# Kernel tuning notes

Hardware: AMD Instinct MI355X
Metric: run time of the kernel (lower is better)

## Reference

```python
import jax, jax.numpy as jnp
import numpy as np

N_HEAD = 16

def setup_inputs() -> dict:
    key = jax.random.key(0)
    k1, k2, k3 = jax.random.split(key, 3)
    B, T, C = 4, 2048, 1024
    x = jax.random.normal(k1, (B, T, C), dtype=jnp.float32)
    W_attn = jax.random.normal(k2, (C, 3 * C), dtype=jnp.float32) * (1.0 / np.sqrt(C))
    b_attn = jnp.zeros((3 * C,), dtype=jnp.float32)
    W_proj = jax.random.normal(k3, (C, C), dtype=jnp.float32) * (1.0 / np.sqrt(C))
    b_proj = jnp.zeros((C,), dtype=jnp.float32)
    return {"x": x, "W_attn": W_attn, "b_attn": b_attn, "W_proj": W_proj, "b_proj": b_proj, "train": 0}

def reference(x, W_attn, b_attn, W_proj, b_proj, train):
    # Causal self-attention, eval mode (dropout = identity since dropout=0.0 / train=False).
    B, T, C = x.shape
    H = N_HEAD
    hd = C // H
    qkv = x @ W_attn + b_attn                      # [B, T, 3C]
    q, k, v = jnp.split(qkv, 3, axis=-1)
    def to_heads(a):
        return a.reshape(B, T, H, hd).swapaxes(1, 2)   # [B, H, T, hd]
    q, k, v = to_heads(q), to_heads(k), to_heads(v)
    scale = 1.0 / jnp.sqrt(jnp.asarray(hd, dtype=x.dtype))
    attn = jnp.einsum('bhqd,bhkd->bhqk', q, k) * scale   # [B, H, T, T]
    causal = jnp.tril(jnp.ones((T, T), dtype=bool))
    attn = jnp.where(causal, attn, -jnp.inf)
    p = jax.nn.softmax(attn, axis=-1)
    y = jnp.einsum('bhqk,bhkd->bhqd', p, v)              # [B, H, T, hd]
    y = y.swapaxes(1, 2).reshape(B, T, C)
    return y @ W_proj + b_proj
```

## Files before the change

### kernel.cpp

```cpp
#include <hip/hip_runtime.h>
#include <hip/hip_bf16.h>
#include <math.h>

typedef __attribute__((ext_vector_type(8))) short short8;
typedef __attribute__((ext_vector_type(4))) short short4v;
typedef __attribute__((ext_vector_type(4))) float floatx4;
using bf16 = __hip_bfloat16;

#define DEVI __device__ __forceinline__

DEVI floatx4 fzero4() { floatx4 z; z[0]=0.f; z[1]=0.f; z[2]=0.f; z[3]=0.f; return z; }

DEVI float ex2(float x) {
  float r;
  asm("v_exp_f32 %0, %1" : "=v"(r) : "v"(x));
  return r;
}

DEVI float max3f(float a, float b, float c) {
  float d;
  asm("v_max3_f32 %0, %1, %2, %3" : "=v"(d) : "v"(a), "v"(b), "v"(c));
  return d;
}

DEVI unsigned short f2b(float x) {
  union { bf16 h; unsigned short u; } c;
  c.h = __float2bfloat16(x);
  return c.u;
}

DEVI floatx4 mfma16(short4v a, short4v b, floatx4 c) {
#if __has_builtin(__builtin_amdgcn_mfma_f32_16x16x16bf16_1k)
  return __builtin_amdgcn_mfma_f32_16x16x16bf16_1k(a, b, c, 0, 0, 0);
#else
  floatx4 d;
  asm("v_mfma_f32_16x16x16_bf16 %0, %1, %2, %3" : "=v"(d) : "v"(a), "v"(b), "v"(c));
  return d;
#endif
}

DEVI void gload16(const bf16* g, bf16* l) {
  typedef __attribute__((address_space(1))) const void gv_t;
  typedef __attribute__((address_space(3))) void lv_t;
  __builtin_amdgcn_global_load_lds((gv_t*)g, (lv_t*)l, 16, 0, 0);
}

__global__ __launch_bounds__(256) void k_transpose(const float* __restrict__ in,
                                                   bf16* __restrict__ out,
                                                   int R, int C) {
  __shared__ float tile[32][33];
  int x = blockIdx.x * 32 + threadIdx.x;
  for (int i = threadIdx.y; i < 32; i += 8) {
    int y = blockIdx.y * 32 + i;
    tile[i][threadIdx.x] = (y < R && x < C) ? in[(size_t)y * C + x] : 0.f;
  }
  __syncthreads();
  int ox = blockIdx.y * 32 + threadIdx.x;
  for (int i = threadIdx.y; i < 32; i += 8) {
    int oy = blockIdx.x * 32 + i;
    if (oy < C && ox < R) out[(size_t)oy * R + ox] = __float2bfloat16(tile[threadIdx.x][i]);
  }
}

#define LOG2E_O8 0.18033688011112042f

__global__ __launch_bounds__(256) void k_gemmA(
    const float* __restrict__ Ax, const bf16* __restrict__ Bt,
    const float* __restrict__ bias,
    bf16* __restrict__ Qo, bf16* __restrict__ Ko, bf16* __restrict__ Vo) {
  __shared__ bf16 sA[2][128 * 32];
  __shared__ bf16 sB[2][128 * 32];
  const int Kd = 1024;
  const int tid = threadIdx.x;
  const int w = tid >> 6, l = tid & 63;
  const int lg = l >> 4, li = l & 15;
  const int wr = w >> 1, wc = w & 1;
  const int ii = blockIdx.x >> 3, xcd = blockIdx.x & 7;
  const int bx = ii >> 3, by = xcd * 8 + (ii & 7);
  const int m0 = by * 128, n0 = bx * 128;

  const int r0 = tid >> 2, ko0 = (tid & 3) * 8;
  const float* pax0 = Ax + (size_t)(m0 + r0) * Kd + ko0;
  const float* pax1 = Ax + (size_t)(m0 + 64 + r0) * Kd + ko0;
  const bf16* pb0 = Bt + (size_t)(n0 + r0) * Kd + ko0;
  const bf16* pb1 = Bt + (size_t)(n0 + 64 + r0) * Kd + ko0;

  floatx4 acc[4][4];
#pragma unroll
  for (int i = 0; i < 4; ++i)
#pragma unroll
    for (int j = 0; j < 4; ++j) acc[i][j] = fzero4();

  float4 va0, va1, va2, va3;

  auto ISSUE_A = [&](int k0) {
    va0 = *(const float4*)(pax0 + k0);
    va1 = *(const float4*)(pax0 + k0 + 4);
    va2 = *(const float4*)(pax1 + k0);
    va3 = *(const float4*)(pax1 + k0 + 4);
  };
  auto WRITE_A = [&](int buf) {
    short8 s0, s1;
    s0[0] = (short)f2b(va0.x); s0[1] = (short)f2b(va0.y);
    s0[2] = (short)f2b(va0.z); s0[3] = (short)f2b(va0.w);
    s0[4] = (short)f2b(va1.x); s0[5] = (short)f2b(va1.y);
    s0[6] = (short)f2b(va1.z); s0[7] = (short)f2b(va1.w);
    s1[0] = (short)f2b(va2.x); s1[1] = (short)f2b(va2.y);
    s1[2] = (short)f2b(va2.z); s1[3] = (short)f2b(va2.w);
    s1[4] = (short)f2b(va3.x); s1[5] = (short)f2b(va3.y);
    s1[6] = (short)f2b(va3.z); s1[7] = (short)f2b(va3.w);
    *(short8*)&sA[buf][r0 * 32 + ko0] = s0;
    *(short8*)&sA[buf][(64 + r0) * 32 + ko0] = s1;
  };
  auto STAGE_B = [&](int buf, int k0) {
    gload16(pb0 + k0, &sB[buf][w * 512]);
    gload16(pb1 + k0, &sB[buf][2048 + w * 512]);
  };

  ISSUE_A(0);
  STAGE_B(0, 0);
  WRITE_A(0);
  asm volatile("s_waitcnt lgkmcnt(0)" ::: "memory");

  int cur = 0;
  for (int k0 = 0; k0 < Kd; k0 += 32) {
    const int nxt = cur ^ 1;
    const bool pf = (k0 + 32 < Kd);
    if (pf) {
      ISSUE_A(k0 + 32);
      STAGE_B(nxt, k0 + 32);
      asm volatile("s_waitcnt vmcnt(6)" ::: "memory");
    } else {
      asm volatile("s_waitcnt vmcnt(0)" ::: "memory");
    }
    __builtin_amdgcn_s_barrier();
    short8 af[4], bfr[4];
#pragma unroll
    for (int i = 0; i < 4; ++i)
      af[i] = *(const short8*)&sA[cur][(wr * 64 + i * 16 + li) * 32 + lg * 8];
#pragma unroll
    for (int j = 0; j < 4; ++j)
      bfr[j] = *(const short8*)&sB[cur][(wc * 64 + j * 16 + li) * 32 + lg * 8];
#pragma unroll
    for (int i = 0; i < 4; ++i)
#pragma unroll
      for (int j = 0; j < 4; ++j)
        acc[i][j] = __builtin_amdgcn_mfma_f32_16x16x32_bf16(af[i], bfr[j], acc[i][j], 0, 0, 0);
    if (pf) {
      WRITE_A(nxt);
      asm volatile("s_waitcnt lgkmcnt(0)" ::: "memory");
    }
    __builtin_amdgcn_s_barrier();
    cur = nxt;
  }

#pragma unroll
  for (int i = 0; i < 4; ++i) {
#pragma unroll
    for (int j = 0; j < 4; ++j) {
      const int ng = n0 + wc * 64 + j * 16 + li;
      const float bs = bias[ng];
      const int mgb = m0 + wr * 64 + i * 16 + lg * 4;
      const int bb = mgb >> 11, t = mgb & 2047;
      const int d = ng & 63;
      if (ng < 1024) {
        const int h = ng >> 6;
#pragma unroll
        for (int r = 0; r < 4; ++r)
          Qo[(((size_t)bb * 16 + h) * 2048 + t + r) * 64 + d] =
              __float2bfloat16((acc[i][j][r] + bs) * LOG2E_O8);
      } else if (ng < 2048) {
        const int h = (ng - 1024) >> 6;
#pragma unroll
        for (int r = 0; r < 4; ++r)
          Ko[(((size_t)bb * 16 + h) * 2048 + t + r) * 64 + d] =
              __float2bfloat16(acc[i][j][r] + bs);
      } else {
        const int h = (ng - 2048) >> 6;
        short4v vv;
#pragma unroll
        for (int r = 0; r < 4; ++r) vv[r] = (short)f2b(acc[i][j][r] + bs);
        *(short4v*)&Vo[(((size_t)bb * 16 + h) * 64 + d) * 2048 + t] = vv;
      }
    }
  }
}

__global__ __launch_bounds__(256) void k_gemm(
    const bf16* __restrict__ A, const bf16* __restrict__ Bt,
    const float* __restrict__ bias, float* __restrict__ Fo, int N, int Kd) {
  __shared__ bf16 sA[2][128 * 32];
  __shared__ bf16 sB[2][128 * 32];
  const int tid = threadIdx.x;
  const int w = tid >> 6, l = tid & 63;
  const int lg = l >> 4, li = l & 15;
  const int wr = w >> 1, wc = w & 1;
  const int ii = blockIdx.x >> 3, xcd = blockIdx.x & 7;
  const int bx = ii >> 3, by = xcd * 8 + (ii & 7);
  const int m0 = by * 128, n0 = bx * 128;

  const int r0 = tid >> 2, ko0 = (tid & 3) * 8;
  const bf16* pa0 = A + (size_t)(m0 + r0) * Kd + ko0;
  const bf16* pa1 = A + (size_t)(m0 + 64 + r0) * Kd + ko0;
  const bf16* pb0 = Bt + (size_t)(n0 + r0) * Kd + ko0;
  const bf16* pb1 = Bt + (size_t)(n0 + 64 + r0) * Kd + ko0;

  floatx4 acc[4][4];
#pragma unroll
  for (int i = 0; i < 4; ++i)
#pragma unroll
    for (int j = 0; j < 4; ++j) acc[i][j] = fzero4();

  auto STAGE = [&](int buf, int k0) {
    gload16(pa0 + k0, &sA[buf][w * 512]);
    gload16(pa1 + k0, &sA[buf][2048 + w * 512]);
    gload16(pb0 + k0, &sB[buf][w * 512]);
    gload16(pb1 + k0, &sB[buf][2048 + w * 512]);
  };

  STAGE(0, 0);
  int cur = 0;
  for (int k0 = 0; k0 < Kd; k0 += 32) {
    if (k0 + 32 < Kd) {
      STAGE(cur ^ 1, k0 + 32);
      asm volatile("s_waitcnt vmcnt(4)" ::: "memory");
    } else {
      asm volatile("s_waitcnt vmcnt(0)" ::: "memory");
    }
    __builtin_amdgcn_s_barrier();
    short8 af[4], bfr[4];
#pragma unroll
    for (int i = 0; i < 4; ++i)
      af[i] = *(const short8*)&sA[cur][(wr * 64 + i * 16 + li) * 32 + lg * 8];
#pragma unroll
    for (int j = 0; j < 4; ++j)
      bfr[j] = *(const short8*)&sB[cur][(wc * 64 + j * 16 + li) * 32 + lg * 8];
#pragma unroll
    for (int i = 0; i < 4; ++i)
#pragma unroll
      for (int j = 0; j < 4; ++j)
        acc[i][j] = __builtin_amdgcn_mfma_f32_16x16x32_bf16(af[i], bfr[j], acc[i][j], 0, 0, 0);
    __builtin_amdgcn_s_barrier();
    cur ^= 1;
  }

#pragma unroll
  for (int i = 0; i < 4; ++i) {
#pragma unroll
    for (int j = 0; j < 4; ++j) {
      const int ng = n0 + wc * 64 + j * 16 + li;
      const float bs = bias[ng];
      const int mgb = m0 + wr * 64 + i * 16 + lg * 4;
#pragma unroll
      for (int r = 0; r < 4; ++r)
        Fo[(size_t)(mgb + r) * N + ng] = acc[i][j][r] + bs;
    }
  }
}

#define T_SEQ 2048

__global__ __launch_bounds__(256) void k_attn(
    const bf16* __restrict__ Q, const bf16* __restrict__ K,
    const bf16* __restrict__ Vt, bf16* __restrict__ Y) {
  __shared__ bf16 sK[2][64 * 64];
  __shared__ bf16 sV[2][64 * 64];

  const int tid = threadIdx.x;
  const int w = tid >> 6, l = tid & 63;
  const int lg = l >> 4, li = l & 15;
  const int bid = blockIdx.x;
  const int sq = bid >> 3;
  const int bh = (bid & 7) * 8 + (sq & 7);
  const int g = sq >> 3;
  const int qd = g >> 2, rr = g & 3;
  const int tb = (qd == 0) ? 15 - rr : (qd == 1) ? 8 + rr : (qd == 2) ? 7 - rr : rr;
  const int b = bh >> 4, h = bh & 15;

  const bf16* Qp = Q + (size_t)bh * (T_SEQ * 64);
  const bf16* Kp = K + (size_t)bh * (T_SEQ * 64);
  const bf16* Vp = Vt + (size_t)bh * (64 * T_SEQ);

  const int q0 = tb * 128;
  const int wq0 = q0 + w * 32;
  const int nst = (q0 + 128) >> 6;

  short8 aq[2][2];
#pragma unroll
  for (int rg = 0; rg < 2; ++rg)
#pragma unroll
    for (int dc = 0; dc < 2; ++dc)
      aq[rg][dc] = *(const short8*)(Qp + (size_t)(wq0 + rg * 16 + li) * 64 + dc * 32 + lg * 8);

  floatx4 o[2][4];
#pragma unroll
  for (int rg = 0; rg < 2; ++rg)
#pragma unroll
    for (int f = 0; f < 4; ++f) o[rg][f] = fzero4();
  float m[2] = {-INFINITY, -INFINITY};
  float lsum[2] = {0.f, 0.f};

  auto STAGE = [&](int buf, int k0) {
#pragma unroll
    for (int half = 0; half < 2; ++half) {
      const int c = half * 256 + tid;
      const int row = c >> 3, cs = c & 7;
      const int sc = cs ^ (row & 7);
      bf16* kb = &sK[buf][(half * 256 + w * 64) * 8];
      bf16* vb = &sV[buf][(half * 256 + w * 64) * 8];
      gload16(Kp + (size_t)(k0 + row) * 64 + sc * 8, kb);
      gload16(Vp + (size_t)row * T_SEQ + k0 + sc * 8, vb);
    }
  };

  int cur = 0;
  STAGE(0, 0);
  for (int t = 0; t < nst; ++t) {
    const int k0 = t << 6;
    if (t + 1 < nst) {
      STAGE(cur ^ 1, k0 + 64);
      asm volatile("s_waitcnt vmcnt(4)" ::: "memory");
    } else {
      asm volatile("s_waitcnt vmcnt(0)" ::: "memory");
    }
    __builtin_amdgcn_s_barrier();
    if (k0 <= wq0 + 31) {
      floatx4 s[2][4];
      __builtin_amdgcn_s_setprio(1);
#pragma unroll
      for (int kt = 0; kt < 4; ++kt) {
        const int rowk = kt * 16 + li;
        const short8 kb0 = *(const short8*)&sK[cur][rowk * 64 + ((lg ^ (rowk & 7)) * 8)];
        const short8 kb1 = *(const short8*)&sK[cur][rowk * 64 + (((4 + lg) ^ (rowk & 7)) * 8)];
#pragma unroll
        for (int rg = 0; rg < 2; ++rg) {
          floatx4 acc = __builtin_amdgcn_mfma_f32_16x16x32_bf16(kb0, aq[rg][0], fzero4(), 0, 0, 0);
          s[rg][kt] = __builtin_amdgcn_mfma_f32_16x16x32_bf16(kb1, aq[rg][1], acc, 0, 0, 0);
        }
      }
      __builtin_amdgcn_s_setprio(0);
      if (k0 + 63 > wq0) {
#pragma unroll
        for (int rg = 0; rg < 2; ++rg) {
          const int qg = wq0 + rg * 16 + li;
#pragma unroll
          for (int kt = 0; kt < 4; ++kt) {
            const int kgb = k0 + kt * 16 + lg * 4;
#pragma unroll
            for (int r = 0; r < 4; ++r)
              if (kgb + r > qg) s[rg][kt][r] = -1e30f;
          }
        }
      }
      float pm[2];
#pragma unroll
      for (int rg = 0; rg < 2; ++rg) {
        float t0 = max3f(s[rg][0][0], s[rg][0][1], s[rg][0][2]);
        float t1 = max3f(s[rg][0][3], s[rg][1][0], s[rg][1][1]);
        float t2 = max3f(s[rg][1][2], s[rg][1][3], s[rg][2][0]);
        float t3 = max3f(s[rg][2][1], s[rg][2][2], s[rg][2][3]);
        float t4 = max3f(s[rg][3][0], s[rg][3][1], s[rg][3][2]);
        float p = fmaxf(max3f(t0, t1, t2), max3f(t3, t4, s[rg][3][3]));
        p = fmaxf(p, __shfl_xor(p, 16));
        p = fmaxf(p, __shfl_xor(p, 32));
        pm[rg] = p;
      }
      const float need = fmaxf(pm[0] - m[0], pm[1] - m[1]);
      if (!__all(need <= 8.0f)) {
#pragma unroll
        for (int rg = 0; rg < 2; ++rg) {
          const float mn = fmaxf(m[rg], pm[rg]);
          const float a = ex2(m[rg] - mn);
          m[rg] = mn;
          lsum[rg] *= a;
          float ar[4];
#pragma unroll
          for (int r = 0; r < 4; ++r) ar[r] = __shfl(a, lg * 4 + r);
#pragma unroll
          for (int f = 0; f < 4; ++f) {
            o[rg][f][0] *= ar[0]; o[rg][f][1] *= ar[1];
            o[rg][f][2] *= ar[2]; o[rg][f][3] *= ar[3];
          }
        }
      }
      short4v pa4[2][4];
#pragma unroll
      for (int rg = 0; rg < 2; ++rg) {
#pragma unroll
        for (int kt = 0; kt < 4; ++kt) {
          const float e0 = ex2(s[rg][kt][0] - m[rg]);
          const float e1 = ex2(s[rg][kt][1] - m[rg]);
          const float e2 = ex2(s[rg][kt][2] - m[rg]);
          const float e3 = ex2(s[rg][kt][3] - m[rg]);
          lsum[rg] += (e0 + e1) + (e2 + e3);
          short4v pv;
          pv[0] = (short)f2b(e0); pv[1] = (short)f2b(e1);
          pv[2] = (short)f2b(e2); pv[3] = (short)f2b(e3);
          pa4[rg][kt] = pv;
        }
      }
      __builtin_amdgcn_s_setprio(1);
#pragma unroll
      for (int f = 0; f < 4; ++f) {
        const int rowv = f * 16 + li;
        const int rx = rowv & 7;
#pragma unroll
        for (int kt = 0; kt < 4; ++kt) {
          const int cc = 2 * kt + (lg >> 1);
          const short4v vb4 = *(const short4v*)&sV[cur][rowv * 64 + (((cc ^ rx) << 3) | ((lg & 1) << 2))];
          o[0][f] = mfma16(pa4[0][kt], vb4, o[0][f]);
          o[1][f] = mfma16(pa4[1][kt], vb4, o[1][f]);
        }
      }
      __builtin_amdgcn_s_setprio(0);
    }
    __builtin_amdgcn_s_barrier();
    cur ^= 1;
  }
#pragma unroll
  for (int rg = 0; rg < 2; ++rg) {
    float Ls = lsum[rg];
    Ls += __shfl_xor(Ls, 16);
    Ls += __shfl_xor(Ls, 32);
#pragma unroll
    for (int r = 0; r < 4; ++r) {
      const float inv = 1.0f / __shfl(Ls, lg * 4 + r);
      const int qg = wq0 + rg * 16 + lg * 4 + r;
      const size_t base = ((size_t)b * T_SEQ + qg) * 1024 + h * 64;
#pragma unroll
      for (int f = 0; f < 4; ++f)
        Y[base + f * 16 + li] = __float2bfloat16(o[rg][f][r] * inv);
    }
  }
}

extern "C" void kernel_launch(void* const* d_in, const int* in_sizes, int n_in,
                              void* d_out, int out_size, void* d_ws, size_t ws_size,
                              hipStream_t stream) {
  const float* x      = (const float*)d_in[0];
  const float* W_attn = (const float*)d_in[1];
  const float* b_attn = (const float*)d_in[2];
  const float* W_proj = (const float*)d_in[3];
  const float* b_proj = (const float*)d_in[4];
  float* out = (float*)d_out;

  char* ws = (char*)d_ws;
  bf16* Wt_a = (bf16*)(ws);
  bf16* Wt_p = (bf16*)(ws + 6291456);
  bf16* Qb   = (bf16*)(ws + 8388608);
  bf16* Kb   = (bf16*)(ws + 25165824);
  bf16* Vtb  = (bf16*)(ws + 41943040);
  bf16* Yb   = (bf16*)(ws + 58720256);

  k_transpose<<<dim3(96, 32), dim3(32, 8), 0, stream>>>(W_attn, Wt_a, 1024, 3072);
  k_transpose<<<dim3(32, 32), dim3(32, 8), 0, stream>>>(W_proj, Wt_p, 1024, 1024);
  k_gemmA<<<1536, 256, 0, stream>>>(x, Wt_a, b_attn, Qb, Kb, Vtb);
  k_attn<<<1024, 256, 0, stream>>>(Qb, Kb, Vtb, Yb);
  k_gemm<<<512, 256, 0, stream>>>(Yb, Wt_p, b_proj, out, 1024, 1024);
}
```

Baseline: 189.6 us.

## Widen attention KV tile from 64 to 128 keys per pipeline stage

Doubles the K/V shared-memory tile to 128 keys per iteration, halving the loop trip count and the barriers and waits per block, with a new 16-chunk XOR swizzle for V rows. It also drops the per-wave causal skip, so every wave processes every tile, including fully masked ones on the diagonal. The cost is double the LDS footprint (64 KB), more registers for scores, and wasted work on masked tiles.

```diff
diff --git a/kernel.cpp b/kernel.cpp
--- a/kernel.cpp
+++ b/kernel.cpp
@@ -263,8 +263,8 @@
 __global__ __launch_bounds__(256) void k_attn(
     const bf16* __restrict__ Q, const bf16* __restrict__ K,
     const bf16* __restrict__ Vt, bf16* __restrict__ Y) {
-  __shared__ bf16 sK[2][64 * 64];
-  __shared__ bf16 sV[2][64 * 64];
+  __shared__ bf16 sK[2][128 * 64];
+  __shared__ bf16 sV[2][64 * 128];
 
   const int tid = threadIdx.x;
   const int w = tid >> 6, l = tid & 63;
@@ -283,7 +283,7 @@
 
   const int q0 = tb * 128;
   const int wq0 = q0 + w * 32;
-  const int nst = (q0 + 128) >> 6;
+  const int nst = tb + 1;
 
   short8 aq[2][2];
 #pragma unroll
@@ -302,33 +302,33 @@
 
   auto STAGE = [&](int buf, int k0) {
 #pragma unroll
-    for (int half = 0; half < 2; ++half) {
-      const int c = half * 256 + tid;
-      const int row = c >> 3, cs = c & 7;
-      const int sc = cs ^ (row & 7);
-      bf16* kb = &sK[buf][(half * 256 + w * 64) * 8];
-      bf16* vb = &sV[buf][(half * 256 + w * 64) * 8];
-      gload16(Kp + (size_t)(k0 + row) * 64 + sc * 8, kb);
-      gload16(Vp + (size_t)row * T_SEQ + k0 + sc * 8, vb);
+    for (int q = 0; q < 4; ++q) {
+      const int c = q * 256 + tid;
+      const int rowK = c >> 3, csK = c & 7;
+      const int scK = csK ^ (rowK & 7);
+      gload16(Kp + (size_t)(k0 + rowK) * 64 + scK * 8, &sK[buf][(q * 256 + w * 64) * 8]);
+      const int rowV = c >> 4, csV = c & 15;
+      const int scV = csV ^ (rowV & 15);
+      gload16(Vp + (size_t)rowV * T_SEQ + k0 + scV * 8, &sV[buf][(q * 256 + w * 64) * 8]);
     }
   };
 
   int cur = 0;
   STAGE(0, 0);
   for (int t = 0; t < nst; ++t) {
-    const int k0 = t << 6;
+    const int k0 = t << 7;
     if (t + 1 < nst) {
-      STAGE(cur ^ 1, k0 + 64);
-      asm volatile("s_waitcnt vmcnt(4)" ::: "memory");
+      STAGE(cur ^ 1, k0 + 128);
+      asm volatile("s_waitcnt vmcnt(8)" ::: "memory");
     } else {
       asm volatile("s_waitcnt vmcnt(0)" ::: "memory");
     }
     __builtin_amdgcn_s_barrier();
-    if (k0 <= wq0 + 31) {
-      floatx4 s[2][4];
+    {
+      floatx4 s[2][8];
       __builtin_amdgcn_s_setprio(1);
 #pragma unroll
-      for (int kt = 0; kt < 4; ++kt) {
+      for (int kt = 0; kt < 8; ++kt) {
         const int rowk = kt * 16 + li;
         const short8 kb0 = *(const short8*)&sK[cur][rowk * 64 + ((lg ^ (rowk & 7)) * 8)];
         const short8 kb1 = *(const short8*)&sK[cur][rowk * 64 + (((4 + lg) ^ (rowk & 7)) * 8)];
@@ -339,12 +339,12 @@
         }
       }
       __builtin_amdgcn_s_setprio(0);
-      if (k0 + 63 > wq0) {
+      if (k0 + 127 > wq0) {
 #pragma unroll
         for (int rg = 0; rg < 2; ++rg) {
           const int qg = wq0 + rg * 16 + li;
 #pragma unroll
-          for (int kt = 0; kt < 4; ++kt) {
+          for (int kt = 0; kt < 8; ++kt) {
             const int kgb = k0 + kt * 16 + lg * 4;
 #pragma unroll
             for (int r = 0; r < 4; ++r)
@@ -355,12 +355,13 @@
       float pm[2];
 #pragma unroll
       for (int rg = 0; rg < 2; ++rg) {
-        float t0 = max3f(s[rg][0][0], s[rg][0][1], s[rg][0][2]);
-        float t1 = max3f(s[rg][0][3], s[rg][1][0], s[rg][1][1]);
-        float t2 = max3f(s[rg][1][2], s[rg][1][3], s[rg][2][0]);
-        float t3 = max3f(s[rg][2][1], s[rg][2][2], s[rg][2][3]);
-        float t4 = max3f(s[rg][3][0], s[rg][3][1], s[rg][3][2]);
-        float p = fmaxf(max3f(t0, t1, t2), max3f(t3, t4, s[rg][3][3]));
+        float mk[8];
+#pragma unroll
+        for (int kt = 0; kt < 8; ++kt)
+          mk[kt] = fmaxf(max3f(s[rg][kt][0], s[rg][kt][1], s[rg][kt][2]), s[rg][kt][3]);
+        float p = max3f(max3f(mk[0], mk[1], mk[2]),
+                        max3f(mk[3], mk[4], mk[5]),
+                        fmaxf(mk[6], mk[7]));
         p = fmaxf(p, __shfl_xor(p, 16));
         p = fmaxf(p, __shfl_xor(p, 32));
         pm[rg] = p;
@@ -383,11 +384,11 @@
           }
         }
       }
-      short4v pa4[2][4];
+      short4v pa4[2][8];
 #pragma unroll
       for (int rg = 0; rg < 2; ++rg) {
 #pragma unroll
-        for (int kt = 0; kt < 4; ++kt) {
+        for (int kt = 0; kt < 8; ++kt) {
           const float e0 = ex2(s[rg][kt][0] - m[rg]);
           const float e1 = ex2(s[rg][kt][1] - m[rg]);
           const float e2 = ex2(s[rg][kt][2] - m[rg]);
@@ -403,11 +404,10 @@
 #pragma unroll
       for (int f = 0; f < 4; ++f) {
         const int rowv = f * 16 + li;
-        const int rx = rowv & 7;
-#pragma unroll
-        for (int kt = 0; kt < 4; ++kt) {
+#pragma unroll
+        for (int kt = 0; kt < 8; ++kt) {
           const int cc = 2 * kt + (lg >> 1);
-          const short4v vb4 = *(const short4v*)&sV[cur][rowv * 64 + (((cc ^ rx) << 3) | ((lg & 1) << 2))];
+          const short4v vb4 = *(const short4v*)&sV[cur][rowv * 128 + (((cc ^ li) << 3) | ((lg & 1) << 2))];
           o[0][f] = mfma16(pa4[0][kt], vb4, o[0][f]);
           o[1][f] = mfma16(pa4[1][kt], vb4, o[1][f]);
         }
```

New measurement: 217.1 us. 1.14x slower.

## Load K/V tiles directly from global per wave instead of LDS staging

Applied to the files above, without the earlier changes.

The attention kernel no longer stages K and V tiles into double-buffered shared memory with block-wide barriers. Each wave now reads its K and V MFMA operands straight from global memory and runs only as many key tiles as its own causal range needs. This removes the LDS writes, the barriers and the block-level loop bound, and frees shared memory, which may allow more blocks per CU. In exchange, all four waves fetch the same tiles separately, raising cache and memory traffic, and there is no explicit prefetch to hide load latency.

```diff
diff --git a/kernel.cpp b/kernel.cpp
--- a/kernel.cpp
+++ b/kernel.cpp
@@ -263,9 +263,6 @@
 __global__ __launch_bounds__(256) void k_attn(
     const bf16* __restrict__ Q, const bf16* __restrict__ K,
     const bf16* __restrict__ Vt, bf16* __restrict__ Y) {
-  __shared__ bf16 sK[2][64 * 64];
-  __shared__ bf16 sV[2][64 * 64];
-
   const int tid = threadIdx.x;
   const int w = tid >> 6, l = tid & 63;
   const int lg = l >> 4, li = l & 15;
@@ -283,7 +280,7 @@
 
   const int q0 = tb * 128;
   const int wq0 = q0 + w * 32;
-  const int nst = (q0 + 128) >> 6;
+  const int nstw = (wq0 >> 6) + 1;
 
   short8 aq[2][2];
 #pragma unroll
@@ -300,122 +297,98 @@
   float m[2] = {-INFINITY, -INFINITY};
   float lsum[2] = {0.f, 0.f};
 
-  auto STAGE = [&](int buf, int k0) {
-#pragma unroll
-    for (int half = 0; half < 2; ++half) {
-      const int c = half * 256 + tid;
-      const int row = c >> 3, cs = c & 7;
-      const int sc = cs ^ (row & 7);
-      bf16* kb = &sK[buf][(half * 256 + w * 64) * 8];
-      bf16* vb = &sV[buf][(half * 256 + w * 64) * 8];
-      gload16(Kp + (size_t)(k0 + row) * 64 + sc * 8, kb);
-      gload16(Vp + (size_t)row * T_SEQ + k0 + sc * 8, vb);
-    }
-  };
-
-  int cur = 0;
-  STAGE(0, 0);
-  for (int t = 0; t < nst; ++t) {
+  for (int t = 0; t < nstw; ++t) {
     const int k0 = t << 6;
-    if (t + 1 < nst) {
-      STAGE(cur ^ 1, k0 + 64);
-      asm volatile("s_waitcnt vmcnt(4)" ::: "memory");
-    } else {
-      asm volatile("s_waitcnt vmcnt(0)" ::: "memory");
-    }
-    __builtin_amdgcn_s_barrier();
-    if (k0 <= wq0 + 31) {
-      floatx4 s[2][4];
-      __builtin_amdgcn_s_setprio(1);
+    short8 kb0[4], kb1[4];
+#pragma unroll
+    for (int kt = 0; kt < 4; ++kt) {
+      const bf16* kp = Kp + (size_t)(k0 + kt * 16 + li) * 64;
+      kb0[kt] = *(const short8*)(kp + lg * 8);
+      kb1[kt] = *(const short8*)(kp + 32 + lg * 8);
+    }
+    floatx4 s[2][4];
+    __builtin_amdgcn_s_setprio(1);
+#pragma unroll
+    for (int kt = 0; kt < 4; ++kt) {
+#pragma unroll
+      for (int rg = 0; rg < 2; ++rg) {
+        floatx4 acc = __builtin_amdgcn_mfma_f32_16x16x32_bf16(kb0[kt], aq[rg][0], fzero4(), 0, 0, 0);
+        s[rg][kt] = __builtin_amdgcn_mfma_f32_16x16x32_bf16(kb1[kt], aq[rg][1], acc, 0, 0, 0);
+      }
+    }
+    __builtin_amdgcn_s_setprio(0);
+    if (k0 + 63 > wq0) {
+#pragma unroll
+      for (int rg = 0; rg < 2; ++rg) {
+        const int qg = wq0 + rg * 16 + li;
+#pragma unroll
+        for (int kt = 0; kt < 4; ++kt) {
+          const int kgb = k0 + kt * 16 + lg * 4;
+#pragma unroll
+          for (int r = 0; r < 4; ++r)
+            if (kgb + r > qg) s[rg][kt][r] = -1e30f;
+        }
+      }
+    }
+    float pm[2];
+#pragma unroll
+    for (int rg = 0; rg < 2; ++rg) {
+      float t0 = max3f(s[rg][0][0], s[rg][0][1], s[rg][0][2]);
+      float t1 = max3f(s[rg][0][3], s[rg][1][0], s[rg][1][1]);
+      float t2 = max3f(s[rg][1][2], s[rg][1][3], s[rg][2][0]);
+      float t3 = max3f(s[rg][2][1], s[rg][2][2], s[rg][2][3]);
+      float t4 = max3f(s[rg][3][0], s[rg][3][1], s[rg][3][2]);
+      float p = fmaxf(max3f(t0, t1, t2), max3f(t3, t4, s[rg][3][3]));
+      p = fmaxf(p, __shfl_xor(p, 16));
+      p = fmaxf(p, __shfl_xor(p, 32));
+      pm[rg] = p;
+    }
+    const float need = fmaxf(pm[0] - m[0], pm[1] - m[1]);
+    if (!__all(need <= 8.0f)) {
+#pragma unroll
+      for (int rg = 0; rg < 2; ++rg) {
+        const float mn = fmaxf(m[rg], pm[rg]);
+        const float a = ex2(m[rg] - mn);
+        m[rg] = mn;
+        lsum[rg] *= a;
+        float ar[4];
+#pragma unroll
+        for (int r = 0; r < 4; ++r) ar[r] = __shfl(a, lg * 4 + r);
+#pragma unroll
+        for (int f = 0; f < 4; ++f) {
+          o[rg][f][0] *= ar[0]; o[rg][f][1] *= ar[1];
+          o[rg][f][2] *= ar[2]; o[rg][f][3] *= ar[3];
+        }
+      }
+    }
+    short4v pa4[2][4];
+#pragma unroll
+    for (int rg = 0; rg < 2; ++rg) {
 #pragma unroll
       for (int kt = 0; kt < 4; ++kt) {
-        const int rowk = kt * 16 + li;
-        const short8 kb0 = *(const short8*)&sK[cur][rowk * 64 + ((lg ^ (rowk & 7)) * 8)];
-        const short8 kb1 = *(const short8*)&sK[cur][rowk * 64 + (((4 + lg) ^ (rowk & 7)) * 8)];
-#pragma unroll
-        for (int rg = 0; rg < 2; ++rg) {
-          floatx4 acc = __builtin_amdgcn_mfma_f32_16x16x32_bf16(kb0, aq[rg][0], fzero4(), 0, 0, 0);
-          s[rg][kt] = __builtin_amdgcn_mfma_f32_16x16x32_bf16(kb1, aq[rg][1], acc, 0, 0, 0);
-        }
-      }
-      __builtin_amdgcn_s_setprio(0);
-      if (k0 + 63 > wq0) {
-#pragma unroll
-        for (int rg = 0; rg < 2; ++rg) {
-          const int qg = wq0 + rg * 16 + li;
-#pragma unroll
-          for (int kt = 0; kt < 4; ++kt) {
-            const int kgb = k0 + kt * 16 + lg * 4;
-#pragma unroll
-            for (int r = 0; r < 4; ++r)
-              if (kgb + r > qg) s[rg][kt][r] = -1e30f;
-          }
-        }
-      }
-      float pm[2];
-#pragma unroll
-      for (int rg = 0; rg < 2; ++rg) {
-        float t0 = max3f(s[rg][0][0], s[rg][0][1], s[rg][0][2]);
-        float t1 = max3f(s[rg][0][3], s[rg][1][0], s[rg][1][1]);
-        float t2 = max3f(s[rg][1][2], s[rg][1][3], s[rg][2][0]);
-        float t3 = max3f(s[rg][2][1], s[rg][2][2], s[rg][2][3]);
-        float t4 = max3f(s[rg][3][0], s[rg][3][1], s[rg][3][2]);
-        float p = fmaxf(max3f(t0, t1, t2), max3f(t3, t4, s[rg][3][3]));
-        p = fmaxf(p, __shfl_xor(p, 16));
-        p = fmaxf(p, __shfl_xor(p, 32));
-        pm[rg] = p;
-      }
-      const float need = fmaxf(pm[0] - m[0], pm[1] - m[1]);
-      if (!__all(need <= 8.0f)) {
-#pragma unroll
-        for (int rg = 0; rg < 2; ++rg) {
-          const float mn = fmaxf(m[rg], pm[rg]);
-          const float a = ex2(m[rg] - mn);
-          m[rg] = mn;
-          lsum[rg] *= a;
-          float ar[4];
-#pragma unroll
-          for (int r = 0; r < 4; ++r) ar[r] = __shfl(a, lg * 4 + r);
-#pragma unroll
-          for (int f = 0; f < 4; ++f) {
-            o[rg][f][0] *= ar[0]; o[rg][f][1] *= ar[1];
-            o[rg][f][2] *= ar[2]; o[rg][f][3] *= ar[3];
-          }
-        }
-      }
-      short4v pa4[2][4];
-#pragma unroll
-      for (int rg = 0; rg < 2; ++rg) {
-#pragma unroll
-        for (int kt = 0; kt < 4; ++kt) {
-          const float e0 = ex2(s[rg][kt][0] - m[rg]);
-          const float e1 = ex2(s[rg][kt][1] - m[rg]);
-          const float e2 = ex2(s[rg][kt][2] - m[rg]);
-          const float e3 = ex2(s[rg][kt][3] - m[rg]);
-          lsum[rg] += (e0 + e1) + (e2 + e3);
-          short4v pv;
-          pv[0] = (short)f2b(e0); pv[1] = (short)f2b(e1);
-          pv[2] = (short)f2b(e2); pv[3] = (short)f2b(e3);
-          pa4[rg][kt] = pv;
-        }
-      }
-      __builtin_amdgcn_s_setprio(1);
-#pragma unroll
-      for (int f = 0; f < 4; ++f) {
-        const int rowv = f * 16 + li;
-        const int rx = rowv & 7;
-#pragma unroll
-        for (int kt = 0; kt < 4; ++kt) {
-          const int cc = 2 * kt + (lg >> 1);
-          const short4v vb4 = *(const short4v*)&sV[cur][rowv * 64 + (((cc ^ rx) << 3) | ((lg & 1) << 2))];
-          o[0][f] = mfma16(pa4[0][kt], vb4, o[0][f]);
-          o[1][f] = mfma16(pa4[1][kt], vb4, o[1][f]);
-        }
-      }
-      __builtin_amdgcn_s_setprio(0);
-    }
-    __builtin_amdgcn_s_barrier();
-    cur ^= 1;
+        const float e0 = ex2(s[rg][kt][0] - m[rg]);
+        const float e1 = ex2(s[rg][kt][1] - m[rg]);
+        const float e2 = ex2(s[rg][kt][2] - m[rg]);
+        const float e3 = ex2(s[rg][kt][3] - m[rg]);
+        lsum[rg] += (e0 + e1) + (e2 + e3);
+        short4v pv;
+        pv[0] = (short)f2b(e0); pv[1] = (short)f2b(e1);
+        pv[2] = (short)f2b(e2); pv[3] = (short)f2b(e3);
+        pa4[rg][kt] = pv;
+      }
+    }
+    __builtin_amdgcn_s_setprio(1);
+#pragma unroll
+    for (int f = 0; f < 4; ++f) {
+      const bf16* vp = Vp + (size_t)(f * 16 + li) * T_SEQ + k0 + lg * 4;
+#pragma unroll
+      for (int kt = 0; kt < 4; ++kt) {
+        const short4v vb4 = *(const short4v*)(vp + kt * 16);
+        o[0][f] = mfma16(pa4[0][kt], vb4, o[0][f]);
+        o[1][f] = mfma16(pa4[1][kt], vb4, o[1][f]);
+      }
+    }
+    __builtin_amdgcn_s_setprio(0);
   }
 #pragma unroll
   for (int rg = 0; rg < 2; ++rg) {
```

Measured after the change: 299.1 us. +57.7%, slower.
